# Kernel optimization log

Hardware: AMD Instinct MI355X
Metric: run time of the kernel (lower is better)

The kernel has to match this reference:

```python
import jax, jax.numpy as jnp
import numpy as np

B, L, D, H = 2, 1024, 1024, 16
HD = D // H  # head_dim = 64
EPS = 1e-12  # F.normalize default eps


def setup_inputs() -> dict:
    key = jax.random.key(0)
    ks = jax.random.split(key, 7)
    s = 1.0 / np.sqrt(D)
    return {
        "x": jax.random.normal(ks[0], (B, L, D), dtype=jnp.float32),
        "Wq": jax.random.normal(ks[1], (D, D), dtype=jnp.float32) * s,
        "Wk": jax.random.normal(ks[2], (D, D), dtype=jnp.float32) * s,
        "Wv": jax.random.normal(ks[3], (D, D), dtype=jnp.float32) * s,
        "Wo": jax.random.normal(ks[4], (D, D), dtype=jnp.float32) * s,
        "Wb": jax.random.normal(ks[5], (D, H), dtype=jnp.float32) * s,
        "bb": jnp.zeros((H,), dtype=jnp.float32),
    }


def _l2norm(t):
    # matches F.normalize(t, dim=-1): t / max(||t||_2, eps)
    n = jnp.sqrt(jnp.sum(t * t, axis=-1, keepdims=True))
    return t / jnp.maximum(n, EPS)


def reference(x, Wq, Wk, Wv, Wo, Wb, bb):
    q = (x @ Wq).reshape(B, L, H, HD)
    k = (x @ Wk).reshape(B, L, H, HD)
    v = (x @ Wv).reshape(B, L, H, HD)
    beta = jax.nn.sigmoid(x @ Wb + bb)          # [B, L, H]
    q = _l2norm(q)
    k = _l2norm(k)
    # gated outer products: [B, L, H, HD, HD]
    kv = jnp.einsum('blhd,blhe->blhde', k, v) * beta[..., None, None]
    kv_cumsum = jnp.cumsum(kv, axis=1)          # causal cumulative kv state
    out = jnp.einsum('blhd,blhde->blhe', q, kv_cumsum)  # [B, L, H, HD]
    return out.reshape(B, L, D) @ Wo
```

## Files before the change

kernel.cpp:

```cpp
#include <hip/hip_runtime.h>
#include <math.h>

#define BB   2
#define LL   1024
#define DD   1024
#define HH   16
#define HDIM 64
#define MM   (BB * LL)
#define CHK  64
#define NCHK (LL / CHK)

typedef short bf16x8 __attribute__((ext_vector_type(8)));
typedef float f32x4  __attribute__((ext_vector_type(4)));
typedef const __attribute__((address_space(1))) unsigned int* gas_ptr;
typedef __attribute__((address_space(3))) unsigned int* las_ptr;

__device__ __forceinline__ void gload16(const void* g, void* l) {
    __builtin_amdgcn_global_load_lds((gas_ptr)(unsigned long long)g,
                                     (las_ptr)(unsigned long long)l, 16, 0, 0);
}

__device__ __forceinline__ unsigned short f2bf(float f) {
    unsigned int u = __float_as_uint(f);
    u += 0x7fffu + ((u >> 16) & 1u);
    return (unsigned short)(u >> 16);
}
__device__ __forceinline__ float bfhi(unsigned int u) { return __uint_as_float(u & 0xffff0000u); }
__device__ __forceinline__ float bflo(unsigned int u) { return __uint_as_float(u << 16); }

__global__ void prep_all(const float* __restrict__ x, unsigned short* __restrict__ xb,
                         const float* __restrict__ Wb, unsigned short* __restrict__ Wbt,
                         const float* __restrict__ W0, const float* __restrict__ W1,
                         const float* __restrict__ W2, const float* __restrict__ W3,
                         unsigned short* __restrict__ T0, unsigned short* __restrict__ T1,
                         unsigned short* __restrict__ T2, unsigned short* __restrict__ T3) {
    const int bid = blockIdx.x;
    if (bid < 2048) {
        const int idx = bid * 256 + threadIdx.x;
        const float4 v = ((const float4*)x)[idx];
        ushort4 o;
        o.x = f2bf(v.x); o.y = f2bf(v.y); o.z = f2bf(v.z); o.w = f2bf(v.w);
        ((ushort4*)xb)[idx] = o;
        return;
    }
    if (bid < 2112) {
        const int t = (bid - 2048) * 256 + threadIdx.x;
        const int h = t >> 10, kidx = t & 1023;
        Wbt[t] = f2bf(Wb[kidx * HH + h]);
        return;
    }
    __shared__ float tile[32][33];
    const int b4 = bid - 2112;
    const int which = b4 >> 10;
    const int b = b4 & 1023;
    const int bk = b >> 5, bn = b & 31;
    const float* W = which == 0 ? W0 : which == 1 ? W1 : which == 2 ? W2 : W3;
    unsigned short* T = which == 0 ? T0 : which == 1 ? T1 : which == 2 ? T2 : T3;
    const int tx = threadIdx.x & 31, ty = threadIdx.x >> 5;
#pragma unroll
    for (int i = 0; i < 4; ++i)
        tile[ty + i * 8][tx] = W[(size_t)(bk * 32 + ty + i * 8) * DD + bn * 32 + tx];
    __syncthreads();
#pragma unroll
    for (int i = 0; i < 4; ++i)
        T[(size_t)(bn * 32 + ty + i * 8) * DD + bk * 32 + tx] = f2bf(tile[tx][ty + i * 8]);
}

__device__ __forceinline__ void gemm_kloop_db(const unsigned short* A, const unsigned short* Bt,
                                              unsigned short* As, unsigned short* Bs,
                                              int rowBase, int colBase, int K,
                                              f32x4 acc[4][4]) {
    const int tid = threadIdx.x;
    const int c0 = tid, c1 = tid + 256;
    const int ar0 = c0 >> 2, ak0 = (c0 & 3) << 3;
    const int ar1 = c1 >> 2, ak1 = (c1 & 3) << 3;
    const unsigned short* Ag0 = A + (size_t)(rowBase + ar0) * K + ak0;
    const unsigned short* Ag1 = A + (size_t)(rowBase + ar1) * K + ak1;
    const unsigned short* Bg0 = Bt + (size_t)(colBase + ar0) * K + ak0;
    const unsigned short* Bg1 = Bt + (size_t)(colBase + ar1) * K + ak1;
    const int lane = tid & 63, wv = tid >> 6;
    const int qr = wv >> 1, qc = wv & 1;
    const int fr = lane & 15;
    const int koff = (lane >> 4) << 3;
    int aoff[4], boff[4];
#pragma unroll
    for (int mi = 0; mi < 4; ++mi) aoff[mi] = (qr * 64 + mi * 16 + fr) * 32 + koff;
#pragma unroll
    for (int nj = 0; nj < 4; ++nj) boff[nj] = (qc * 64 + nj * 16 + fr) * 32 + koff;

    gload16(Ag0, As + c0 * 8); gload16(Ag1, As + c1 * 8);
    gload16(Bg0, Bs + c0 * 8); gload16(Bg1, Bs + c1 * 8);
    Ag0 += 32; Ag1 += 32; Bg0 += 32; Bg1 += 32;

    for (int k0 = 0; k0 < K; k0 += 32) {
        const int cur = (k0 >> 5) & 1;
        const int nxt = cur ^ 1;
        __syncthreads();
        if (k0 + 32 < K) {
            gload16(Ag0, As + nxt * 4096 + c0 * 8); gload16(Ag1, As + nxt * 4096 + c1 * 8);
            gload16(Bg0, Bs + nxt * 4096 + c0 * 8); gload16(Bg1, Bs + nxt * 4096 + c1 * 8);
            Ag0 += 32; Ag1 += 32; Bg0 += 32; Bg1 += 32;
        }
        const unsigned short* Ab = As + cur * 4096;
        const unsigned short* Bb = Bs + cur * 4096;
        bf16x8 av[4], bv[4];
#pragma unroll
        for (int mi = 0; mi < 4; ++mi) av[mi] = *(const bf16x8*)(Ab + aoff[mi]);
#pragma unroll
        for (int nj = 0; nj < 4; ++nj) bv[nj] = *(const bf16x8*)(Bb + boff[nj]);
#pragma unroll
        for (int mi = 0; mi < 4; ++mi)
#pragma unroll
            for (int nj = 0; nj < 4; ++nj)
                acc[mi][nj] = __builtin_amdgcn_mfma_f32_16x16x32_bf16(av[mi], bv[nj], acc[mi][nj], 0, 0, 0);
    }
}

__global__ __launch_bounds__(256) void gemm_qkv_beta(const unsigned short* __restrict__ xb,
                                                     const unsigned short* __restrict__ Wqt,
                                                     const unsigned short* __restrict__ Wkt,
                                                     const unsigned short* __restrict__ Wvt,
                                                     const unsigned short* __restrict__ Wbt,
                                                     const float* __restrict__ bbp,
                                                     unsigned short* __restrict__ qb,
                                                     unsigned short* __restrict__ kb,
                                                     unsigned short* __restrict__ vb,
                                                     float* __restrict__ beta) {
    __shared__ unsigned short As[2 * 128 * 32];
    __shared__ unsigned short Bs[2 * 128 * 32];
    const int lane = threadIdx.x & 63, wv = threadIdx.x >> 6;
    const int fr = lane & 15, quad = lane >> 4;
    if (blockIdx.x >= 384) {
        const int rowBase = (blockIdx.x - 384) * 128;
        const int r0 = rowBase + wv * 32 + fr;
        f32x4 bacc[2];
        bacc[0] = (f32x4){0.f, 0.f, 0.f, 0.f};
        bacc[1] = (f32x4){0.f, 0.f, 0.f, 0.f};
        for (int k0 = 0; k0 < DD; k0 += 32) {
            const int kk = k0 + quad * 8;
            const bf16x8 a0 = *(const bf16x8*)&xb[(size_t)r0 * DD + kk];
            const bf16x8 a1 = *(const bf16x8*)&xb[(size_t)(r0 + 16) * DD + kk];
            const bf16x8 bw = *(const bf16x8*)&Wbt[(size_t)fr * DD + kk];
            bacc[0] = __builtin_amdgcn_mfma_f32_16x16x32_bf16(a0, bw, bacc[0], 0, 0, 0);
            bacc[1] = __builtin_amdgcn_mfma_f32_16x16x32_bf16(a1, bw, bacc[1], 0, 0, 0);
        }
        const float bias = bbp[fr];
#pragma unroll
        for (int mi = 0; mi < 2; ++mi)
#pragma unroll
            for (int i = 0; i < 4; ++i) {
                const int row = rowBase + wv * 32 + mi * 16 + quad * 4 + i;
                const float s = bacc[mi][i] + bias;
                beta[row * HH + fr] = 1.0f / (1.0f + expf(-s));
            }
        return;
    }
    const int by = blockIdx.x / 24, bxx = blockIdx.x % 24;
    const int mat = bxx >> 3, tn = bxx & 7;
    const unsigned short* Bt = mat == 0 ? Wqt : (mat == 1 ? Wkt : Wvt);
    unsigned short* Cout = mat == 0 ? qb : (mat == 1 ? kb : vb);
    f32x4 acc[4][4];
#pragma unroll
    for (int mi = 0; mi < 4; ++mi)
#pragma unroll
        for (int nj = 0; nj < 4; ++nj) acc[mi][nj] = (f32x4){0.f, 0.f, 0.f, 0.f};
    gemm_kloop_db(xb, Bt, As, Bs, by * 128, tn * 128, DD, acc);

    const int qr = wv >> 1, qc = wv & 1;
    if (mat < 2) {
#pragma unroll
        for (int mi = 0; mi < 4; ++mi)
#pragma unroll
            for (int i = 0; i < 4; ++i) {
                float s = 0.f;
#pragma unroll
                for (int nj = 0; nj < 4; ++nj) { float t = acc[mi][nj][i]; s += t * t; }
                s += __shfl_xor(s, 1, 64);
                s += __shfl_xor(s, 2, 64);
                s += __shfl_xor(s, 4, 64);
                s += __shfl_xor(s, 8, 64);
                const float inv = 1.0f / fmaxf(sqrtf(s), 1e-12f);
#pragma unroll
                for (int nj = 0; nj < 4; ++nj) acc[mi][nj][i] *= inv;
            }
    }
#pragma unroll
    for (int mi = 0; mi < 4; ++mi)
#pragma unroll
        for (int i = 0; i < 4; ++i) {
            const int row = by * 128 + qr * 64 + mi * 16 + quad * 4 + i;
#pragma unroll
            for (int nj = 0; nj < 4; ++nj) {
                const int col = tn * 128 + qc * 64 + nj * 16 + fr;
                Cout[(size_t)row * DD + col] = f2bf(acc[mi][nj][i]);
            }
        }
}

__global__ __launch_bounds__(256) void chunkkv_kernel(const unsigned short* __restrict__ k,
                                                      const unsigned short* __restrict__ v,
                                                      const float* __restrict__ beta,
                                                      unsigned short* __restrict__ states) {
    const int c = blockIdx.x % NCHK;
    const int bh = blockIdx.x / NCHK;
    const int b = bh / HH, h = bh % HH;
    __shared__ __align__(16) unsigned short kT[64 * 72];
    __shared__ __align__(16) unsigned short vT[64 * 72];
    __shared__ __align__(16) unsigned short tT[64 * 72];
    const int tid = threadIdx.x;
    for (int i = tid; i < 512; i += 256) {
        const int t = i >> 3, dg = (i & 7) << 3;
        const int m = b * LL + c * CHK + t;
        const float be = beta[m * HH + h];
        const size_t go = (size_t)m * DD + h * 64 + dg;
        const uint4 ku = *(const uint4*)&k[go];
        const uint4 vu = *(const uint4*)&v[go];
        unsigned int kw[4] = {ku.x, ku.y, ku.z, ku.w};
        unsigned int vw[4] = {vu.x, vu.y, vu.z, vu.w};
#pragma unroll
        for (int jj = 0; jj < 4; ++jj) {
            kT[(dg + 2 * jj)     * 72 + t] = f2bf(bflo(kw[jj]) * be);
            kT[(dg + 2 * jj + 1) * 72 + t] = f2bf(bfhi(kw[jj]) * be);
            vT[(dg + 2 * jj)     * 72 + t] = (unsigned short)(vw[jj] & 0xffffu);
            vT[(dg + 2 * jj + 1) * 72 + t] = (unsigned short)(vw[jj] >> 16);
        }
    }
    __syncthreads();
    const int lane = tid & 63, wv = tid >> 6;
    const int fr = lane & 15, quad = lane >> 4;
    f32x4 acc[4];
#pragma unroll
    for (int et = 0; et < 4; ++et) acc[et] = (f32x4){0.f, 0.f, 0.f, 0.f};
#pragma unroll
    for (int kh = 0; kh < 2; ++kh) {
        const int tc = kh * 32 + quad * 8;
        const bf16x8 a = *(const bf16x8*)&kT[(wv * 16 + fr) * 72 + tc];
#pragma unroll
        for (int et = 0; et < 4; ++et) {
            const bf16x8 bb = *(const bf16x8*)&vT[(et * 16 + fr) * 72 + tc];
            acc[et] = __builtin_amdgcn_mfma_f32_16x16x32_bf16(a, bb, acc[et], 0, 0, 0);
        }
    }
#pragma unroll
    for (int et = 0; et < 4; ++et)
#pragma unroll
        for (int i = 0; i < 4; ++i)
            tT[(et * 16 + fr) * 72 + wv * 16 + quad * 4 + i] = f2bf(acc[et][i]);
    __syncthreads();
    unsigned short* outp = states + ((size_t)bh * NCHK + c) * 4096;
#pragma unroll
    for (int s = 0; s < 2; ++s) {
        const int p = tid * 16 + s * 8;
        const int e = p >> 6, d = p & 63;
        *(uint4*)&outp[p] = *(const uint4*)&tT[e * 72 + d];
    }
}

__global__ __launch_bounds__(256) void attn_kernel(const unsigned short* __restrict__ q,
                                                   const unsigned short* __restrict__ k,
                                                   const unsigned short* __restrict__ v,
                                                   const float* __restrict__ beta,
                                                   const unsigned short* __restrict__ states,
                                                   unsigned short* __restrict__ y) {
    const int c = blockIdx.x % NCHK;
    const int bh = blockIdx.x / NCHK;
    const int b = bh / HH, h = bh % HH;
    __shared__ __align__(16) unsigned short qS[64 * 80];
    __shared__ __align__(16) unsigned short kS[64 * 80];
    __shared__ __align__(16) unsigned short sS[64 * 80];
    __shared__ __align__(16) unsigned short vT[64 * 72];
    __shared__ __align__(16) unsigned short sT[64 * 72];
    const int tid = threadIdx.x;
    for (int i = tid; i < 512; i += 256) {
        const int t = i >> 3, dg = (i & 7) << 3;
        const int m = b * LL + c * CHK + t;
        const float be = beta[m * HH + h];
        const size_t go = (size_t)m * DD + h * 64 + dg;
        const uint4 qu = *(const uint4*)&q[go];
        const uint4 ku = *(const uint4*)&k[go];
        const uint4 vu = *(const uint4*)&v[go];
        *(uint4*)&qS[t * 80 + dg] = qu;
        *(uint4*)&kS[t * 80 + dg] = ku;
        unsigned int vw[4] = {vu.x, vu.y, vu.z, vu.w};
#pragma unroll
        for (int jj = 0; jj < 4; ++jj) {
            vT[(dg + 2 * jj)     * 72 + t] = f2bf(bflo(vw[jj]) * be);
            vT[(dg + 2 * jj + 1) * 72 + t] = f2bf(bfhi(vw[jj]) * be);
        }
    }
    {
        float racc[16];
#pragma unroll
        for (int j = 0; j < 16; ++j) racc[j] = 0.f;
        const unsigned short* sbase = states + (size_t)bh * NCHK * 4096;
        const int p0 = tid * 16;
        for (int cc = 0; cc < c; ++cc) {
            const uint4 u0 = *(const uint4*)&sbase[cc * 4096 + p0];
            const uint4 u1 = *(const uint4*)&sbase[cc * 4096 + p0 + 8];
            const unsigned int w[8] = {u0.x, u0.y, u0.z, u0.w, u1.x, u1.y, u1.z, u1.w};
#pragma unroll
            for (int j = 0; j < 8; ++j) {
                racc[2 * j]     += bflo(w[j]);
                racc[2 * j + 1] += bfhi(w[j]);
            }
        }
        const int e = p0 >> 6, d0 = p0 & 63;
#pragma unroll
        for (int j = 0; j < 16; ++j)
            sT[e * 72 + d0 + j] = f2bf(racc[j]);
    }
    __syncthreads();
    const int lane = tid & 63, wv = tid >> 6;
    const int fr = lane & 15, quad = lane >> 4;
    const int koff = quad * 8;
    f32x4 s_acc[4];
#pragma unroll
    for (int j = 0; j < 4; ++j) s_acc[j] = (f32x4){0.f, 0.f, 0.f, 0.f};
#pragma unroll
    for (int kh = 0; kh < 2; ++kh) {
        const bf16x8 a = *(const bf16x8*)&qS[(wv * 16 + fr) * 80 + kh * 32 + koff];
#pragma unroll
        for (int j = 0; j < 4; ++j) {
            const bf16x8 bb = *(const bf16x8*)&kS[(j * 16 + fr) * 80 + kh * 32 + koff];
            s_acc[j] = __builtin_amdgcn_mfma_f32_16x16x32_bf16(a, bb, s_acc[j], 0, 0, 0);
        }
    }
#pragma unroll
    for (int j = 0; j < 4; ++j)
#pragma unroll
        for (int i = 0; i < 4; ++i) {
            const int t = wv * 16 + quad * 4 + i;
            const int s = j * 16 + fr;
            sS[t * 80 + s] = (s <= t) ? f2bf(s_acc[j][i]) : (unsigned short)0;
        }
    f32x4 o_acc[4];
#pragma unroll
    for (int j = 0; j < 4; ++j) o_acc[j] = (f32x4){0.f, 0.f, 0.f, 0.f};
#pragma unroll
    for (int kh = 0; kh < 2; ++kh) {
        const bf16x8 a = *(const bf16x8*)&sS[(wv * 16 + fr) * 80 + kh * 32 + koff];
#pragma unroll
        for (int j = 0; j < 4; ++j) {
            const bf16x8 bb = *(const bf16x8*)&vT[(j * 16 + fr) * 72 + kh * 32 + koff];
            o_acc[j] = __builtin_amdgcn_mfma_f32_16x16x32_bf16(a, bb, o_acc[j], 0, 0, 0);
        }
    }
#pragma unroll
    for (int kh = 0; kh < 2; ++kh) {
        const bf16x8 a = *(const bf16x8*)&qS[(wv * 16 + fr) * 80 + kh * 32 + koff];
#pragma unroll
        for (int j = 0; j < 4; ++j) {
            const bf16x8 bb = *(const bf16x8*)&sT[(j * 16 + fr) * 72 + kh * 32 + koff];
            o_acc[j] = __builtin_amdgcn_mfma_f32_16x16x32_bf16(a, bb, o_acc[j], 0, 0, 0);
        }
    }
#pragma unroll
    for (int j = 0; j < 4; ++j)
#pragma unroll
        for (int i = 0; i < 4; ++i) {
            const int m = b * LL + c * CHK + wv * 16 + quad * 4 + i;
            const int e = j * 16 + fr;
            y[(size_t)m * DD + h * 64 + e] = f2bf(o_acc[j][i]);
        }
}

__global__ __launch_bounds__(256) void gemm_out(const unsigned short* __restrict__ yb,
                                                const unsigned short* __restrict__ Wot,
                                                float* __restrict__ out) {
    __shared__ unsigned short As[2 * 64 * 32];
    __shared__ unsigned short Bs[2 * 128 * 32];
    const int by = blockIdx.x >> 3, tn = blockIdx.x & 7;
    const int tid = threadIdx.x;
    const int rowBase = by * 64, colBase = tn * 128;
    const int ar = tid >> 2, ak = (tid & 3) << 3;
    const unsigned short* Ag = yb + (size_t)(rowBase + ar) * DD + ak;
    const int c1 = tid + 256;
    const int br1 = c1 >> 2, bk1 = (c1 & 3) << 3;
    const unsigned short* Bg0 = Wot + (size_t)(colBase + ar) * DD + ak;
    const unsigned short* Bg1 = Wot + (size_t)(colBase + br1) * DD + bk1;
    const int lane = tid & 63, wv = tid >> 6;
    const int rh = wv & 1, ch = wv >> 1;
    const int fr = lane & 15, koff = (lane >> 4) << 3;
    int aoff[2], boff[4];
#pragma unroll
    for (int mi = 0; mi < 2; ++mi) aoff[mi] = (rh * 32 + mi * 16 + fr) * 32 + koff;
#pragma unroll
    for (int nj = 0; nj < 4; ++nj) boff[nj] = (ch * 64 + nj * 16 + fr) * 32 + koff;
    f32x4 acc[2][4];
#pragma unroll
    for (int mi = 0; mi < 2; ++mi)
#pragma unroll
        for (int nj = 0; nj < 4; ++nj) acc[mi][nj] = (f32x4){0.f, 0.f, 0.f, 0.f};

    gload16(Ag, As + tid * 8);
    gload16(Bg0, Bs + tid * 8); gload16(Bg1, Bs + c1 * 8);
    Ag += 32; Bg0 += 32; Bg1 += 32;

    for (int k0 = 0; k0 < DD; k0 += 32) {
        const int cur = (k0 >> 5) & 1;
        const int nxt = cur ^ 1;
        __syncthreads();
        if (k0 + 32 < DD) {
            gload16(Ag, As + nxt * 2048 + tid * 8);
            gload16(Bg0, Bs + nxt * 4096 + tid * 8); gload16(Bg1, Bs + nxt * 4096 + c1 * 8);
            Ag += 32; Bg0 += 32; Bg1 += 32;
        }
        const unsigned short* Ab = As + cur * 2048;
        const unsigned short* Bb = Bs + cur * 4096;
        bf16x8 av[2], bv[4];
#pragma unroll
        for (int mi = 0; mi < 2; ++mi) av[mi] = *(const bf16x8*)(Ab + aoff[mi]);
#pragma unroll
        for (int nj = 0; nj < 4; ++nj) bv[nj] = *(const bf16x8*)(Bb + boff[nj]);
#pragma unroll
        for (int mi = 0; mi < 2; ++mi)
#pragma unroll
            for (int nj = 0; nj < 4; ++nj)
                acc[mi][nj] = __builtin_amdgcn_mfma_f32_16x16x32_bf16(av[mi], bv[nj], acc[mi][nj], 0, 0, 0);
    }
    const int quad = lane >> 4;
#pragma unroll
    for (int mi = 0; mi < 2; ++mi)
#pragma unroll
        for (int i = 0; i < 4; ++i) {
            const int row = rowBase + rh * 32 + mi * 16 + quad * 4 + i;
#pragma unroll
            for (int nj = 0; nj < 4; ++nj) {
                const int col = colBase + ch * 64 + nj * 16 + fr;
                out[(size_t)row * DD + col] = acc[mi][nj][i];
            }
        }
}

extern "C" void kernel_launch(void* const* d_in, const int* in_sizes, int n_in,
                              void* d_out, int out_size, void* d_ws, size_t ws_size,
                              hipStream_t stream) {
    (void)in_sizes; (void)n_in; (void)out_size; (void)ws_size;
    const float* x  = (const float*)d_in[0];
    const float* Wq = (const float*)d_in[1];
    const float* Wk = (const float*)d_in[2];
    const float* Wv = (const float*)d_in[3];
    const float* Wo = (const float*)d_in[4];
    const float* Wb = (const float*)d_in[5];
    const float* bbp = (const float*)d_in[6];
    float* out = (float*)d_out;

    char* ws = (char*)d_ws;
    unsigned short* xb  = (unsigned short*)ws;                      ws += (size_t)MM * DD * 2;
    unsigned short* Wqt = (unsigned short*)ws;                      ws += (size_t)DD * DD * 2;
    unsigned short* Wkt = (unsigned short*)ws;                      ws += (size_t)DD * DD * 2;
    unsigned short* Wvt = (unsigned short*)ws;                      ws += (size_t)DD * DD * 2;
    unsigned short* Wot = (unsigned short*)ws;                      ws += (size_t)DD * DD * 2;
    unsigned short* Wbt = (unsigned short*)ws;                      ws += (size_t)HH * DD * 2;
    unsigned short* qb  = (unsigned short*)ws;                      ws += (size_t)MM * DD * 2;
    unsigned short* kb  = (unsigned short*)ws;                      ws += (size_t)MM * DD * 2;
    unsigned short* vb  = (unsigned short*)ws;                      ws += (size_t)MM * DD * 2;
    unsigned short* yb  = (unsigned short*)ws;                      ws += (size_t)MM * DD * 2;
    float*          beta   = (float*)ws;                            ws += (size_t)MM * HH * 4;
    unsigned short* states = (unsigned short*)ws;                   ws += (size_t)BB * HH * NCHK * 4096 * 2;

    prep_all<<<6208, 256, 0, stream>>>(x, xb, Wb, Wbt, Wq, Wk, Wv, Wo, Wqt, Wkt, Wvt, Wot);
    gemm_qkv_beta<<<400, 256, 0, stream>>>(xb, Wqt, Wkt, Wvt, Wbt, bbp, qb, kb, vb, beta);
    chunkkv_kernel<<<BB * HH * NCHK, 256, 0, stream>>>(kb, vb, beta, states);
    attn_kernel<<<BB * HH * NCHK, 256, 0, stream>>>(qb, kb, vb, beta, states, yb);
    gemm_out<<<32 * 8, 256, 0, stream>>>(yb, Wot, out);
}
```

Measured before the change: 134.4 us.

## Fuse chunk state computation into attention kernel and widen GEMM k-tiles to 64

Removes the separate chunk-KV state kernel and its global states buffer; each attention block now recomputes the prefix state by looping over all earlier chunks with MFMA, accumulating in registers. Both GEMMs switch to a 64-wide k-tile with double buffering, halving barrier count per k. QKV GEMM now assumes contiguous Wq/Wk/Wv and q/k/v workspace layouts via pointer offsets. The attention change trades one launch and a states round-trip for redundant, triangular work (later chunks reload up to 15 chunks of k/v), creating load imbalance.

New measurement: 158.6 us. 1.18x slower.

```diff
diff --git a/kernel.cpp b/kernel.cpp
--- a/kernel.cpp
+++ b/kernel.cpp
@@ -66,69 +66,16 @@
         T[(size_t)(bn * 32 + ty + i * 8) * DD + bk * 32 + tx] = f2bf(tile[tx][ty + i * 8]);
 }
 
-__device__ __forceinline__ void gemm_kloop_db(const unsigned short* A, const unsigned short* Bt,
-                                              unsigned short* As, unsigned short* Bs,
-                                              int rowBase, int colBase, int K,
-                                              f32x4 acc[4][4]) {
-    const int tid = threadIdx.x;
-    const int c0 = tid, c1 = tid + 256;
-    const int ar0 = c0 >> 2, ak0 = (c0 & 3) << 3;
-    const int ar1 = c1 >> 2, ak1 = (c1 & 3) << 3;
-    const unsigned short* Ag0 = A + (size_t)(rowBase + ar0) * K + ak0;
-    const unsigned short* Ag1 = A + (size_t)(rowBase + ar1) * K + ak1;
-    const unsigned short* Bg0 = Bt + (size_t)(colBase + ar0) * K + ak0;
-    const unsigned short* Bg1 = Bt + (size_t)(colBase + ar1) * K + ak1;
-    const int lane = tid & 63, wv = tid >> 6;
-    const int qr = wv >> 1, qc = wv & 1;
-    const int fr = lane & 15;
-    const int koff = (lane >> 4) << 3;
-    int aoff[4], boff[4];
-#pragma unroll
-    for (int mi = 0; mi < 4; ++mi) aoff[mi] = (qr * 64 + mi * 16 + fr) * 32 + koff;
-#pragma unroll
-    for (int nj = 0; nj < 4; ++nj) boff[nj] = (qc * 64 + nj * 16 + fr) * 32 + koff;
-
-    gload16(Ag0, As + c0 * 8); gload16(Ag1, As + c1 * 8);
-    gload16(Bg0, Bs + c0 * 8); gload16(Bg1, Bs + c1 * 8);
-    Ag0 += 32; Ag1 += 32; Bg0 += 32; Bg1 += 32;
-
-    for (int k0 = 0; k0 < K; k0 += 32) {
-        const int cur = (k0 >> 5) & 1;
-        const int nxt = cur ^ 1;
-        __syncthreads();
-        if (k0 + 32 < K) {
-            gload16(Ag0, As + nxt * 4096 + c0 * 8); gload16(Ag1, As + nxt * 4096 + c1 * 8);
-            gload16(Bg0, Bs + nxt * 4096 + c0 * 8); gload16(Bg1, Bs + nxt * 4096 + c1 * 8);
-            Ag0 += 32; Ag1 += 32; Bg0 += 32; Bg1 += 32;
-        }
-        const unsigned short* Ab = As + cur * 4096;
-        const unsigned short* Bb = Bs + cur * 4096;
-        bf16x8 av[4], bv[4];
-#pragma unroll
-        for (int mi = 0; mi < 4; ++mi) av[mi] = *(const bf16x8*)(Ab + aoff[mi]);
-#pragma unroll
-        for (int nj = 0; nj < 4; ++nj) bv[nj] = *(const bf16x8*)(Bb + boff[nj]);
-#pragma unroll
-        for (int mi = 0; mi < 4; ++mi)
-#pragma unroll
-            for (int nj = 0; nj < 4; ++nj)
-                acc[mi][nj] = __builtin_amdgcn_mfma_f32_16x16x32_bf16(av[mi], bv[nj], acc[mi][nj], 0, 0, 0);
-    }
-}
-
 __global__ __launch_bounds__(256) void gemm_qkv_beta(const unsigned short* __restrict__ xb,
                                                      const unsigned short* __restrict__ Wqt,
-                                                     const unsigned short* __restrict__ Wkt,
-                                                     const unsigned short* __restrict__ Wvt,
                                                      const unsigned short* __restrict__ Wbt,
                                                      const float* __restrict__ bbp,
-                                                     unsigned short* __restrict__ qb,
-                                                     unsigned short* __restrict__ kb,
-                                                     unsigned short* __restrict__ vb,
+                                                     unsigned short* __restrict__ qkv,
                                                      float* __restrict__ beta) {
-    __shared__ unsigned short As[2 * 128 * 32];
-    __shared__ unsigned short Bs[2 * 128 * 32];
-    const int lane = threadIdx.x & 63, wv = threadIdx.x >> 6;
+    __shared__ unsigned short As[2 * 128 * 64];
+    __shared__ unsigned short Bs[2 * 128 * 64];
+    const int tid = threadIdx.x;
+    const int lane = tid & 63, wv = tid >> 6;
     const int fr = lane & 15, quad = lane >> 4;
     if (blockIdx.x >= 384) {
         const int rowBase = (blockIdx.x - 384) * 128;
@@ -157,16 +104,57 @@
     }
     const int by = blockIdx.x / 24, bxx = blockIdx.x % 24;
     const int mat = bxx >> 3, tn = bxx & 7;
-    const unsigned short* Bt = mat == 0 ? Wqt : (mat == 1 ? Wkt : Wvt);
-    unsigned short* Cout = mat == 0 ? qb : (mat == 1 ? kb : vb);
+    const unsigned short* Bt = Wqt + (size_t)mat * DD * DD;
+    unsigned short* Cout = qkv + (size_t)mat * MM * DD;
+    const int rowBase = by * 128, colBase = tn * 128;
+    const int srow = tid >> 3, scol = (tid & 7) << 3;
+    const unsigned short* Ag = xb + (size_t)(rowBase + srow) * DD + scol;
+    const unsigned short* Bg = Bt + (size_t)(colBase + srow) * DD + scol;
+    const int sdst = tid * 8;
+    const int qr = wv >> 1, qc = wv & 1;
+    const int koff = quad << 3;
+    int aoff[4], boff[4];
+#pragma unroll
+    for (int mi = 0; mi < 4; ++mi) aoff[mi] = (qr * 64 + mi * 16 + fr) * 64 + koff;
+#pragma unroll
+    for (int nj = 0; nj < 4; ++nj) boff[nj] = (qc * 64 + nj * 16 + fr) * 64 + koff;
     f32x4 acc[4][4];
 #pragma unroll
     for (int mi = 0; mi < 4; ++mi)
 #pragma unroll
         for (int nj = 0; nj < 4; ++nj) acc[mi][nj] = (f32x4){0.f, 0.f, 0.f, 0.f};
-    gemm_kloop_db(xb, Bt, As, Bs, by * 128, tn * 128, DD, acc);
-
-    const int qr = wv >> 1, qc = wv & 1;
+
+#pragma unroll
+    for (int j = 0; j < 4; ++j) {
+        gload16(Ag + (size_t)j * 32 * DD, As + j * 2048 + sdst);
+        gload16(Bg + (size_t)j * 32 * DD, Bs + j * 2048 + sdst);
+    }
+    for (int k0 = 0; k0 < DD; k0 += 64) {
+        const int cur = (k0 >> 6) & 1, nxt = cur ^ 1;
+        __syncthreads();
+        if (k0 + 64 < DD) {
+#pragma unroll
+            for (int j = 0; j < 4; ++j) {
+                gload16(Ag + k0 + 64 + (size_t)j * 32 * DD, As + nxt * 8192 + j * 2048 + sdst);
+                gload16(Bg + k0 + 64 + (size_t)j * 32 * DD, Bs + nxt * 8192 + j * 2048 + sdst);
+            }
+        }
+        const unsigned short* Ab = As + cur * 8192;
+        const unsigned short* Bb = Bs + cur * 8192;
+#pragma unroll
+        for (int ks = 0; ks < 2; ++ks) {
+            bf16x8 av[4], bv[4];
+#pragma unroll
+            for (int mi = 0; mi < 4; ++mi) av[mi] = *(const bf16x8*)(Ab + aoff[mi] + ks * 32);
+#pragma unroll
+            for (int nj = 0; nj < 4; ++nj) bv[nj] = *(const bf16x8*)(Bb + boff[nj] + ks * 32);
+#pragma unroll
+            for (int mi = 0; mi < 4; ++mi)
+#pragma unroll
+                for (int nj = 0; nj < 4; ++nj)
+                    acc[mi][nj] = __builtin_amdgcn_mfma_f32_16x16x32_bf16(av[mi], bv[nj], acc[mi][nj], 0, 0, 0);
+        }
+    }
     if (mat < 2) {
 #pragma unroll
         for (int mi = 0; mi < 4; ++mi)
@@ -188,79 +176,19 @@
     for (int mi = 0; mi < 4; ++mi)
 #pragma unroll
         for (int i = 0; i < 4; ++i) {
-            const int row = by * 128 + qr * 64 + mi * 16 + quad * 4 + i;
+            const int row = rowBase + qr * 64 + mi * 16 + quad * 4 + i;
 #pragma unroll
             for (int nj = 0; nj < 4; ++nj) {
-                const int col = tn * 128 + qc * 64 + nj * 16 + fr;
+                const int col = colBase + qc * 64 + nj * 16 + fr;
                 Cout[(size_t)row * DD + col] = f2bf(acc[mi][nj][i]);
             }
         }
-}
-
-__global__ __launch_bounds__(256) void chunkkv_kernel(const unsigned short* __restrict__ k,
-                                                      const unsigned short* __restrict__ v,
-                                                      const float* __restrict__ beta,
-                                                      unsigned short* __restrict__ states) {
-    const int c = blockIdx.x % NCHK;
-    const int bh = blockIdx.x / NCHK;
-    const int b = bh / HH, h = bh % HH;
-    __shared__ __align__(16) unsigned short kT[64 * 72];
-    __shared__ __align__(16) unsigned short vT[64 * 72];
-    __shared__ __align__(16) unsigned short tT[64 * 72];
-    const int tid = threadIdx.x;
-    for (int i = tid; i < 512; i += 256) {
-        const int t = i >> 3, dg = (i & 7) << 3;
-        const int m = b * LL + c * CHK + t;
-        const float be = beta[m * HH + h];
-        const size_t go = (size_t)m * DD + h * 64 + dg;
-        const uint4 ku = *(const uint4*)&k[go];
-        const uint4 vu = *(const uint4*)&v[go];
-        unsigned int kw[4] = {ku.x, ku.y, ku.z, ku.w};
-        unsigned int vw[4] = {vu.x, vu.y, vu.z, vu.w};
-#pragma unroll
-        for (int jj = 0; jj < 4; ++jj) {
-            kT[(dg + 2 * jj)     * 72 + t] = f2bf(bflo(kw[jj]) * be);
-            kT[(dg + 2 * jj + 1) * 72 + t] = f2bf(bfhi(kw[jj]) * be);
-            vT[(dg + 2 * jj)     * 72 + t] = (unsigned short)(vw[jj] & 0xffffu);
-            vT[(dg + 2 * jj + 1) * 72 + t] = (unsigned short)(vw[jj] >> 16);
-        }
-    }
-    __syncthreads();
-    const int lane = tid & 63, wv = tid >> 6;
-    const int fr = lane & 15, quad = lane >> 4;
-    f32x4 acc[4];
-#pragma unroll
-    for (int et = 0; et < 4; ++et) acc[et] = (f32x4){0.f, 0.f, 0.f, 0.f};
-#pragma unroll
-    for (int kh = 0; kh < 2; ++kh) {
-        const int tc = kh * 32 + quad * 8;
-        const bf16x8 a = *(const bf16x8*)&kT[(wv * 16 + fr) * 72 + tc];
-#pragma unroll
-        for (int et = 0; et < 4; ++et) {
-            const bf16x8 bb = *(const bf16x8*)&vT[(et * 16 + fr) * 72 + tc];
-            acc[et] = __builtin_amdgcn_mfma_f32_16x16x32_bf16(a, bb, acc[et], 0, 0, 0);
-        }
-    }
-#pragma unroll
-    for (int et = 0; et < 4; ++et)
-#pragma unroll
-        for (int i = 0; i < 4; ++i)
-            tT[(et * 16 + fr) * 72 + wv * 16 + quad * 4 + i] = f2bf(acc[et][i]);
-    __syncthreads();
-    unsigned short* outp = states + ((size_t)bh * NCHK + c) * 4096;
-#pragma unroll
-    for (int s = 0; s < 2; ++s) {
-        const int p = tid * 16 + s * 8;
-        const int e = p >> 6, d = p & 63;
-        *(uint4*)&outp[p] = *(const uint4*)&tT[e * 72 + d];
-    }
 }
 
 __global__ __launch_bounds__(256) void attn_kernel(const unsigned short* __restrict__ q,
                                                    const unsigned short* __restrict__ k,
                                                    const unsigned short* __restrict__ v,
                                                    const float* __restrict__ beta,
-                                                   const unsigned short* __restrict__ states,
                                                    unsigned short* __restrict__ y) {
     const int c = blockIdx.x % NCHK;
     const int bh = blockIdx.x / NCHK;
@@ -271,6 +199,52 @@
     __shared__ __align__(16) unsigned short vT[64 * 72];
     __shared__ __align__(16) unsigned short sT[64 * 72];
     const int tid = threadIdx.x;
+    const int lane = tid & 63, wv = tid >> 6;
+    const int fr = lane & 15, quad = lane >> 4;
+    const int koff = quad * 8;
+    unsigned short* kP = qS;
+    unsigned short* vP = kS;
+
+    f32x4 st_acc[4];
+#pragma unroll
+    for (int et = 0; et < 4; ++et) st_acc[et] = (f32x4){0.f, 0.f, 0.f, 0.f};
+    for (int cc = 0; cc < c; ++cc) {
+        __syncthreads();
+        for (int i = tid; i < 512; i += 256) {
+            const int t = i >> 3, dg = (i & 7) << 3;
+            const int m = b * LL + cc * CHK + t;
+            const float be = beta[m * HH + h];
+            const size_t go = (size_t)m * DD + h * 64 + dg;
+            const uint4 ku = *(const uint4*)&k[go];
+            const uint4 vu = *(const uint4*)&v[go];
+            const unsigned int kw[4] = {ku.x, ku.y, ku.z, ku.w};
+            const unsigned int vw[4] = {vu.x, vu.y, vu.z, vu.w};
+#pragma unroll
+            for (int jj = 0; jj < 4; ++jj) {
+                kP[(dg + 2 * jj)     * 72 + t] = f2bf(bflo(kw[jj]) * be);
+                kP[(dg + 2 * jj + 1) * 72 + t] = f2bf(bfhi(kw[jj]) * be);
+                vP[(dg + 2 * jj)     * 72 + t] = (unsigned short)(vw[jj] & 0xffffu);
+                vP[(dg + 2 * jj + 1) * 72 + t] = (unsigned short)(vw[jj] >> 16);
+            }
+        }
+        __syncthreads();
+#pragma unroll
+        for (int kh = 0; kh < 2; ++kh) {
+            const bf16x8 a = *(const bf16x8*)&kP[(wv * 16 + fr) * 72 + kh * 32 + koff];
+#pragma unroll
+            for (int et = 0; et < 4; ++et) {
+                const bf16x8 bb = *(const bf16x8*)&vP[(et * 16 + fr) * 72 + kh * 32 + koff];
+                st_acc[et] = __builtin_amdgcn_mfma_f32_16x16x32_bf16(a, bb, st_acc[et], 0, 0, 0);
+            }
+        }
+    }
+#pragma unroll
+    for (int et = 0; et < 4; ++et)
+#pragma unroll
+        for (int i = 0; i < 4; ++i)
+            sT[(et * 16 + fr) * 72 + wv * 16 + quad * 4 + i] = f2bf(st_acc[et][i]);
+    __syncthreads();
+
     for (int i = tid; i < 512; i += 256) {
         const int t = i >> 3, dg = (i & 7) << 3;
         const int m = b * LL + c * CHK + t;
@@ -281,38 +255,14 @@
         const uint4 vu = *(const uint4*)&v[go];
         *(uint4*)&qS[t * 80 + dg] = qu;
         *(uint4*)&kS[t * 80 + dg] = ku;
-        unsigned int vw[4] = {vu.x, vu.y, vu.z, vu.w};
+        const unsigned int vw[4] = {vu.x, vu.y, vu.z, vu.w};
 #pragma unroll
         for (int jj = 0; jj < 4; ++jj) {
             vT[(dg + 2 * jj)     * 72 + t] = f2bf(bflo(vw[jj]) * be);
             vT[(dg + 2 * jj + 1) * 72 + t] = f2bf(bfhi(vw[jj]) * be);
         }
     }
-    {
-        float racc[16];
-#pragma unroll
-        for (int j = 0; j < 16; ++j) racc[j] = 0.f;
-        const unsigned short* sbase = states + (size_t)bh * NCHK * 4096;
-        const int p0 = tid * 16;
-        for (int cc = 0; cc < c; ++cc) {
-            const uint4 u0 = *(const uint4*)&sbase[cc * 4096 + p0];
-            const uint4 u1 = *(const uint4*)&sbase[cc * 4096 + p0 + 8];
-            const unsigned int w[8] = {u0.x, u0.y, u0.z, u0.w, u1.x, u1.y, u1.z, u1.w};
-#pragma unroll
-            for (int j = 0; j < 8; ++j) {
-                racc[2 * j]     += bflo(w[j]);
-                racc[2 * j + 1] += bfhi(w[j]);
-            }
-        }
-        const int e = p0 >> 6, d0 = p0 & 63;
-#pragma unroll
-        for (int j = 0; j < 16; ++j)
-            sT[e * 72 + d0 + j] = f2bf(racc[j]);
-    }
     __syncthreads();
-    const int lane = tid & 63, wv = tid >> 6;
-    const int fr = lane & 15, quad = lane >> 4;
-    const int koff = quad * 8;
     f32x4 s_acc[4];
 #pragma unroll
     for (int j = 0; j < 4; ++j) s_acc[j] = (f32x4){0.f, 0.f, 0.f, 0.f};
@@ -367,58 +317,64 @@
 __global__ __launch_bounds__(256) void gemm_out(const unsigned short* __restrict__ yb,
                                                 const unsigned short* __restrict__ Wot,
                                                 float* __restrict__ out) {
-    __shared__ unsigned short As[2 * 64 * 32];
-    __shared__ unsigned short Bs[2 * 128 * 32];
+    __shared__ unsigned short As[2 * 64 * 64];
+    __shared__ unsigned short Bs[2 * 128 * 64];
     const int by = blockIdx.x >> 3, tn = blockIdx.x & 7;
     const int tid = threadIdx.x;
     const int rowBase = by * 64, colBase = tn * 128;
-    const int ar = tid >> 2, ak = (tid & 3) << 3;
-    const unsigned short* Ag = yb + (size_t)(rowBase + ar) * DD + ak;
-    const int c1 = tid + 256;
-    const int br1 = c1 >> 2, bk1 = (c1 & 3) << 3;
-    const unsigned short* Bg0 = Wot + (size_t)(colBase + ar) * DD + ak;
-    const unsigned short* Bg1 = Wot + (size_t)(colBase + br1) * DD + bk1;
+    const int srow = tid >> 3, scol = (tid & 7) << 3;
+    const unsigned short* Ag = yb + (size_t)(rowBase + srow) * DD + scol;
+    const unsigned short* Bg = Wot + (size_t)(colBase + srow) * DD + scol;
+    const int sdst = tid * 8;
     const int lane = tid & 63, wv = tid >> 6;
     const int rh = wv & 1, ch = wv >> 1;
-    const int fr = lane & 15, koff = (lane >> 4) << 3;
+    const int fr = lane & 15, quad = lane >> 4;
+    const int koff = quad << 3;
     int aoff[2], boff[4];
 #pragma unroll
-    for (int mi = 0; mi < 2; ++mi) aoff[mi] = (rh * 32 + mi * 16 + fr) * 32 + koff;
-#pragma unroll
-    for (int nj = 0; nj < 4; ++nj) boff[nj] = (ch * 64 + nj * 16 + fr) * 32 + koff;
+    for (int mi = 0; mi < 2; ++mi) aoff[mi] = (rh * 32 + mi * 16 + fr) * 64 + koff;
+#pragma unroll
+    for (int nj = 0; nj < 4; ++nj) boff[nj] = (ch * 64 + nj * 16 + fr) * 64 + koff;
     f32x4 acc[2][4];
 #pragma unroll
     for (int mi = 0; mi < 2; ++mi)
 #pragma unroll
         for (int nj = 0; nj < 4; ++nj) acc[mi][nj] = (f32x4){0.f, 0.f, 0.f, 0.f};
 
-    gload16(Ag, As + tid * 8);
-    gload16(Bg0, Bs + tid * 8); gload16(Bg1, Bs + c1 * 8);
-    Ag += 32; Bg0 += 32; Bg1 += 32;
-
-    for (int k0 = 0; k0 < DD; k0 += 32) {
-        const int cur = (k0 >> 5) & 1;
-        const int nxt = cur ^ 1;
+#pragma unroll
+    for (int j = 0; j < 2; ++j)
+        gload16(Ag + (size_t)j * 32 * DD, As + j * 2048 + sdst);
+#pragma unroll
+    for (int j = 0; j < 4; ++j)
+        gload16(Bg + (size_t)j * 32 * DD, Bs + j * 2048 + sdst);
+
+    for (int k0 = 0; k0 < DD; k0 += 64) {
+        const int cur = (k0 >> 6) & 1, nxt = cur ^ 1;
         __syncthreads();
-        if (k0 + 32 < DD) {
-            gload16(Ag, As + nxt * 2048 + tid * 8);
-            gload16(Bg0, Bs + nxt * 4096 + tid * 8); gload16(Bg1, Bs + nxt * 4096 + c1 * 8);
-            Ag += 32; Bg0 += 32; Bg1 += 32;
-        }
-        const unsigned short* Ab = As + cur * 2048;
-        const unsigned short* Bb = Bs + cur * 4096;
-        bf16x8 av[2], bv[4];
-#pragma unroll
-        for (int mi = 0; mi < 2; ++mi) av[mi] = *(const bf16x8*)(Ab + aoff[mi]);
-#pragma unroll
-        for (int nj = 0; nj < 4; ++nj) bv[nj] = *(const bf16x8*)(Bb + boff[nj]);
-#pragma unroll
-        for (int mi = 0; mi < 2; ++mi)
-#pragma unroll
-            for (int nj = 0; nj < 4; ++nj)
-                acc[mi][nj] = __builtin_amdgcn_mfma_f32_16x16x32_bf16(av[mi], bv[nj], acc[mi][nj], 0, 0, 0);
-    }
-    const int quad = lane >> 4;
+        if (k0 + 64 < DD) {
+#pragma unroll
+            for (int j = 0; j < 2; ++j)
+                gload16(Ag + k0 + 64 + (size_t)j * 32 * DD, As + nxt * 4096 + j * 2048 + sdst);
+#pragma unroll
+            for (int j = 0; j < 4; ++j)
+                gload16(Bg + k0 + 64 + (size_t)j * 32 * DD, Bs + nxt * 8192 + j * 2048 + sdst);
+        }
+        const unsigned short* Ab = As + cur * 4096;
+        const unsigned short* Bb = Bs + cur * 8192;
+#pragma unroll
+        for (int ks = 0; ks < 2; ++ks) {
+            bf16x8 av[2], bv[4];
+#pragma unroll
+            for (int mi = 0; mi < 2; ++mi) av[mi] = *(const bf16x8*)(Ab + aoff[mi] + ks * 32);
+#pragma unroll
+            for (int nj = 0; nj < 4; ++nj) bv[nj] = *(const bf16x8*)(Bb + boff[nj] + ks * 32);
+#pragma unroll
+            for (int mi = 0; mi < 2; ++mi)
+#pragma unroll
+                for (int nj = 0; nj < 4; ++nj)
+                    acc[mi][nj] = __builtin_amdgcn_mfma_f32_16x16x32_bf16(av[mi], bv[nj], acc[mi][nj], 0, 0, 0);
+        }
+    }
 #pragma unroll
     for (int mi = 0; mi < 2; ++mi)
 #pragma unroll
@@ -457,11 +413,9 @@
     unsigned short* vb  = (unsigned short*)ws;                      ws += (size_t)MM * DD * 2;
     unsigned short* yb  = (unsigned short*)ws;                      ws += (size_t)MM * DD * 2;
     float*          beta   = (float*)ws;                            ws += (size_t)MM * HH * 4;
-    unsigned short* states = (unsigned short*)ws;                   ws += (size_t)BB * HH * NCHK * 4096 * 2;
 
     prep_all<<<6208, 256, 0, stream>>>(x, xb, Wb, Wbt, Wq, Wk, Wv, Wo, Wqt, Wkt, Wvt, Wot);
-    gemm_qkv_beta<<<400, 256, 0, stream>>>(xb, Wqt, Wkt, Wvt, Wbt, bbp, qb, kb, vb, beta);
-    chunkkv_kernel<<<BB * HH * NCHK, 256, 0, stream>>>(kb, vb, beta, states);
-    attn_kernel<<<BB * HH * NCHK, 256, 0, stream>>>(qb, kb, vb, beta, states, yb);
+    gemm_qkv_beta<<<400, 256, 0, stream>>>(xb, Wqt, Wbt, bbp, qb, beta);
+    attn_kernel<<<BB * HH * NCHK, 256, 0, stream>>>(qb, kb, vb, beta, yb);
     gemm_out<<<32 * 8, 256, 0, stream>>>(yb, Wot, out);
 }
```
